# Kernel tuning notes

Measured on AMD Instinct MI355X. Metric: run time of the kernel, lower is better.

The kernel has to match this reference:

```python
import jax, jax.numpy as jnp
import numpy as np

TOPK_RATIO = 0.8


def setup_inputs() -> dict:
    key = jax.random.key(0)
    k1, k2, k3 = jax.random.split(key, 3)
    B, N, C = 32, 1024, 256
    x = jax.random.normal(k1, (B, N, C), dtype=jnp.float32)
    A = jax.random.uniform(k2, (B, N, N), dtype=jnp.float32)
    W = jax.random.normal(k3, (1, C), dtype=jnp.float32)  # nn.Linear(C, 1, bias=False).weight
    mask = jnp.ones((B, N), dtype=bool)                   # all nodes valid
    N_nodes = jnp.full((B,), N, dtype=jnp.int32)          # params_dict['N_nodes']
    return {"x": x, "A": A, "W": W, "mask": mask, "N_nodes": N_nodes}


def reference(x, A, W, mask, N_nodes):
    B, N, C = x.shape
    mask_f = mask.astype(x.dtype)
    n_nodes_f = N_nodes.astype(x.dtype)

    # unsup attention: alpha = normalize(exp(x @ W^T) * mask)
    alpha = jnp.exp(jnp.einsum('bnc,oc->bn', x, W)) * mask_f      # (B, N)
    alpha = alpha / (jnp.sum(alpha, axis=1, keepdims=True) + 1e-7)

    x = x * alpha[:, :, None]
    if N > 700:  # static shape condition, matches torch branch
        x = x * n_nodes_f[:, None, None]

    # top-k pooling: zero the mask of the N_remove lowest-alpha (valid) nodes
    N_remove = jnp.round(n_nodes_f * (1.0 - TOPK_RATIO)).astype(jnp.int32)  # (B,)
    order = jnp.argsort(alpha, axis=1)          # ascending alpha
    rank = jnp.argsort(order, axis=1)           # ascending rank per node
    new_mask = mask & (rank >= N_remove[:, None])  # all nodes valid => rank over valid set

    # drop_nodes_edges: gather the K kept nodes (static K since mask is full)
    K = N - int(round(N * (1.0 - TOPK_RATIO)))  # 819 for N=1024
    # score ranks valid nodes above invalid, earlier index first among valid
    score = new_mask.astype(jnp.int32) * (N + 1) - jnp.arange(N, dtype=jnp.int32)[None, :]
    _, idx = jax.lax.top_k(score, K)            # (B, K) kept node indices
    mask_kept = jnp.take_along_axis(new_mask, idx, axis=1)            # (B, K)
    x = jnp.take_along_axis(x, idx[:, :, None], axis=1)               # (B, K, C)
    A = jnp.take_along_axis(A, idx[:, :, None], axis=1)               # (B, K, N)
    A = jnp.take_along_axis(A, idx[:, None, :], axis=2)               # (B, K, K)

    mask_matrix = mask_kept[:, :, None] & mask_kept[:, None, :]
    A = A * mask_matrix.astype(A.dtype)
    return x, A, mask_kept, alpha
```

## Files before the change

### kernel.cpp

```cpp
#include <hip/hip_runtime.h>

#define B 32
#define N 1024
#define C 256
#define K 819
#define RPB 4
#define NROWGRP 205

__global__ __launch_bounds__(256) void k1_scores(const float* __restrict__ x,
                                                 const float* __restrict__ W,
                                                 float* __restrict__ y) {
    int row  = blockIdx.x * 4 + (threadIdx.x >> 6);
    int lane = threadIdx.x & 63;
    if (row >= B * N) return;
    const float4 xv = ((const float4*)(x + (size_t)row * C))[lane];
    const float4 wv = ((const float4*)W)[lane];
    float s = xv.x * wv.x + xv.y * wv.y + xv.z * wv.z + xv.w * wv.w;
    #pragma unroll
    for (int off = 32; off >= 1; off >>= 1)
        s += __shfl_down(s, off);
    if (lane == 0) y[row] = expf(s);
}

__global__ __launch_bounds__(1024) void k2_select(const float* __restrict__ y,
                                                  const int* __restrict__ N_nodes,
                                                  int* __restrict__ idx,
                                                  float* __restrict__ scale,
                                                  float* __restrict__ out_alpha,
                                                  float* __restrict__ out_mask) {
    __shared__ float a_sh[N];
    __shared__ float red[16];
    __shared__ int   wcnt[16];
    const int b    = blockIdx.x;
    const int i    = threadIdx.x;
    const int w    = i >> 6;
    const int lane = i & 63;

    float yi = y[b * N + i];

    float s = yi;
    #pragma unroll
    for (int off = 32; off >= 1; off >>= 1)
        s += __shfl_down(s, off);
    if (lane == 0) red[w] = s;
    __syncthreads();
    if (i == 0) {
        float S = 0.f;
        #pragma unroll
        for (int k = 0; k < 16; k++) S += red[k];
        red[0] = S + 1e-7f;
    }
    __syncthreads();
    const float denom = red[0];
    const float ai = yi / denom;
    a_sh[i] = ai;
    out_alpha[b * N + i] = ai;
    __syncthreads();

    int cnt = 0;
    for (int j = 0; j < N; j++) {
        float aj = a_sh[j];
        cnt += (int)((aj < ai) | ((aj == ai) & (j < i)));
    }

    const float nf = (float)N_nodes[b];
    const int nrem = (int)rintf(nf * (float)(1.0 - 0.8));
    const bool kept = (cnt >= nrem);

    unsigned long long bal = __ballot(kept);
    if (lane == 0) wcnt[w] = __popcll(bal);
    __syncthreads();
    int woff = 0;
    for (int k = 0; k < w; k++) woff += wcnt[k];
    if (kept) {
        int pos = woff + __popcll(bal & ((1ull << lane) - 1ull));
        idx[b * K + pos]      = i;
        scale[b * K + pos]    = ai * nf;
        out_mask[b * K + pos] = 1.0f;
    }
}

__global__ __launch_bounds__(256) void k3_gather_x(const float* __restrict__ x,
                                                   const int* __restrict__ idx,
                                                   const float* __restrict__ scale,
                                                   float* __restrict__ out_x) {
    const int bk = blockIdx.x;
    const int c  = threadIdx.x;
    const int b  = bk / K;
    const int node  = idx[bk];
    const float sc  = scale[bk];
    out_x[(size_t)bk * C + c] = x[((size_t)b * N + node) * C + c] * sc;
}

__global__ __launch_bounds__(256) void k4_gather_A(const float* __restrict__ A,
                                                   const int* __restrict__ idx,
                                                   float* __restrict__ out_A) {
    __shared__ int   idx_sh[K];
    __shared__ float rows[RPB][N];
    const int t  = threadIdx.x;
    const int b  = blockIdx.x / NROWGRP;
    const int i0 = (blockIdx.x % NROWGRP) * RPB;

    for (int j = t; j < K; j += 256) idx_sh[j] = idx[b * K + j];
    __syncthreads();

    #pragma unroll
    for (int r = 0; r < RPB; r++) {
        int i = i0 + r;
        if (i < K) {
            const float4* rp = (const float4*)(A + ((size_t)b * N + idx_sh[i]) * N);
            ((float4*)rows[r])[t] = rp[t];
        }
    }
    __syncthreads();

    #pragma unroll
    for (int r = 0; r < RPB; r++) {
        int i = i0 + r;
        if (i < K) {
            float* op = out_A + ((size_t)b * K + i) * K;
            for (int j = t; j < K; j += 256) op[j] = rows[r][idx_sh[j]];
        }
    }
}

extern "C" void kernel_launch(void* const* d_in, const int* in_sizes, int n_in,
                              void* d_out, int out_size, void* d_ws, size_t ws_size,
                              hipStream_t stream) {
    const float* x  = (const float*)d_in[0];
    const float* A  = (const float*)d_in[1];
    const float* W  = (const float*)d_in[2];
    const int* N_nodes = (const int*)d_in[4];

    float* out = (float*)d_out;
    const size_t x_sz = (size_t)B * K * C;
    const size_t A_sz = (size_t)B * K * K;
    const size_t m_sz = (size_t)B * K;
    float* out_x     = out;
    float* out_A     = out + x_sz;
    float* out_mask  = out + x_sz + A_sz;
    float* out_alpha = out + x_sz + A_sz + m_sz;

    float* y     = (float*)d_ws;
    int*   idx   = (int*)(y + (size_t)B * N);
    float* scale = (float*)(idx + (size_t)B * K);

    k1_scores<<<(B * N) / 4, 256, 0, stream>>>(x, W, y);
    k2_select<<<B, 1024, 0, stream>>>(y, N_nodes, idx, scale, out_alpha, out_mask);
    k3_gather_x<<<B * K, 256, 0, stream>>>(x, idx, scale, out_x);
    k4_gather_A<<<B * NROWGRP, 256, 0, stream>>>(A, idx, out_A);
}
```

Before: 301.3 us.

## Split ranking across more blocks and fuse x gather into A gather kernel

The single-block-per-batch select kernel is split in two. A rank kernel uses 4 blocks per batch and ranks on the raw exp scores, writing ballot bitmasks plus the per-batch sum. A small emit kernel then computes alpha and compacts the kept indices. The separate x-gather kernel, which used one tiny block per row, is folded into the A-gather kernel, and rows per block rise from 4 to 8. This adds a kernel launch and relies on ranking raw scores giving the same order as normalized alpha.

```diff
diff --git a/kernel.cpp b/kernel.cpp
--- a/kernel.cpp
+++ b/kernel.cpp
@@ -4,15 +4,14 @@
 #define N 1024
 #define C 256
 #define K 819
-#define RPB 4
-#define NROWGRP 205
+#define RPB 8
+#define NROWGRP 103
 
-__global__ __launch_bounds__(256) void k1_scores(const float* __restrict__ x,
+__global__ __launch_bounds__(256) void kA_scores(const float* __restrict__ x,
                                                  const float* __restrict__ W,
                                                  float* __restrict__ y) {
     int row  = blockIdx.x * 4 + (threadIdx.x >> 6);
     int lane = threadIdx.x & 63;
-    if (row >= B * N) return;
     const float4 xv = ((const float4*)(x + (size_t)row * C))[lane];
     const float4 wv = ((const float4*)W)[lane];
     float s = xv.x * wv.x + xv.y * wv.y + xv.z * wv.z + xv.w * wv.w;
@@ -22,101 +21,123 @@
     if (lane == 0) y[row] = expf(s);
 }
 
-__global__ __launch_bounds__(1024) void k2_select(const float* __restrict__ y,
-                                                  const int* __restrict__ N_nodes,
-                                                  int* __restrict__ idx,
-                                                  float* __restrict__ scale,
-                                                  float* __restrict__ out_alpha,
-                                                  float* __restrict__ out_mask) {
-    __shared__ float a_sh[N];
-    __shared__ float red[16];
-    __shared__ int   wcnt[16];
-    const int b    = blockIdx.x;
-    const int i    = threadIdx.x;
-    const int w    = i >> 6;
-    const int lane = i & 63;
+__global__ __launch_bounds__(256) void kB_rank(const float* __restrict__ y,
+                                               const int* __restrict__ N_nodes,
+                                               unsigned long long* __restrict__ bits,
+                                               float* __restrict__ denom) {
+    __shared__ float ysh[N];
+    __shared__ float red[4];
+    const int q = blockIdx.x;
+    const int b = blockIdx.y;
+    const int t = threadIdx.x;
+    const int w = t >> 6, lane = t & 63;
 
-    float yi = y[b * N + i];
-
-    float s = yi;
-    #pragma unroll
-    for (int off = 32; off >= 1; off >>= 1)
-        s += __shfl_down(s, off);
-    if (lane == 0) red[w] = s;
-    __syncthreads();
-    if (i == 0) {
-        float S = 0.f;
-        #pragma unroll
-        for (int k = 0; k < 16; k++) S += red[k];
-        red[0] = S + 1e-7f;
-    }
-    __syncthreads();
-    const float denom = red[0];
-    const float ai = yi / denom;
-    a_sh[i] = ai;
-    out_alpha[b * N + i] = ai;
+    ((float4*)ysh)[t] = ((const float4*)(y + (size_t)b * N))[t];
     __syncthreads();
 
+    const int i = q * 256 + t;
+    const float yi = ysh[i];
     int cnt = 0;
+    #pragma unroll 8
     for (int j = 0; j < N; j++) {
-        float aj = a_sh[j];
-        cnt += (int)((aj < ai) | ((aj == ai) & (j < i)));
+        float yj = ysh[j];
+        cnt += (int)((yj < yi) | ((yj == yi) & (j < i)));
     }
 
     const float nf = (float)N_nodes[b];
-    const int nrem = (int)rintf(nf * (float)(1.0 - 0.8));
+    const int nrem = (int)rintf(nf * 0.2f);
     const bool kept = (cnt >= nrem);
 
     unsigned long long bal = __ballot(kept);
-    if (lane == 0) wcnt[w] = __popcll(bal);
+    if (lane == 0) bits[b * 16 + q * 4 + w] = bal;
+
+    if (q == 0) {
+        float s = ysh[t] + ysh[t + 256] + ysh[t + 512] + ysh[t + 768];
+        #pragma unroll
+        for (int off = 32; off >= 1; off >>= 1)
+            s += __shfl_down(s, off);
+        if (lane == 0) red[w] = s;
+        __syncthreads();
+        if (t == 0) denom[b] = (red[0] + red[1] + red[2] + red[3]) + 1e-7f;
+    }
+}
+
+__global__ __launch_bounds__(1024) void kC_emit(const float* __restrict__ y,
+                                                const unsigned long long* __restrict__ bits,
+                                                const float* __restrict__ denom,
+                                                const int* __restrict__ N_nodes,
+                                                int* __restrict__ idx,
+                                                float* __restrict__ scale,
+                                                float* __restrict__ out_alpha,
+                                                float* __restrict__ out_mask) {
+    __shared__ unsigned long long w_sh[16];
+    __shared__ int c_sh[16];
+    const int b = blockIdx.x;
+    const int i = threadIdx.x;
+    if (i < 16) {
+        unsigned long long wv = bits[b * 16 + i];
+        w_sh[i] = wv;
+        c_sh[i] = __popcll(wv);
+    }
     __syncthreads();
-    int woff = 0;
-    for (int k = 0; k < w; k++) woff += wcnt[k];
-    if (kept) {
-        int pos = woff + __popcll(bal & ((1ull << lane) - 1ull));
+
+    const float d  = denom[b];
+    const float ai = y[b * N + i] / d;
+    out_alpha[b * N + i] = ai;
+
+    const int w = i >> 6, l = i & 63;
+    if ((w_sh[w] >> l) & 1ull) {
+        int pos = __popcll(w_sh[w] & ((1ull << l) - 1ull));
+        for (int k = 0; k < w; k++) pos += c_sh[k];
+        const float nf = (float)N_nodes[b];
         idx[b * K + pos]      = i;
         scale[b * K + pos]    = ai * nf;
         out_mask[b * K + pos] = 1.0f;
     }
 }
 
-__global__ __launch_bounds__(256) void k3_gather_x(const float* __restrict__ x,
-                                                   const int* __restrict__ idx,
-                                                   const float* __restrict__ scale,
-                                                   float* __restrict__ out_x) {
-    const int bk = blockIdx.x;
-    const int c  = threadIdx.x;
-    const int b  = bk / K;
-    const int node  = idx[bk];
-    const float sc  = scale[bk];
-    out_x[(size_t)bk * C + c] = x[((size_t)b * N + node) * C + c] * sc;
-}
-
-__global__ __launch_bounds__(256) void k4_gather_A(const float* __restrict__ A,
-                                                   const int* __restrict__ idx,
-                                                   float* __restrict__ out_A) {
+__global__ __launch_bounds__(256) void kD_gather(const float* __restrict__ A,
+                                                 const float* __restrict__ x,
+                                                 const int* __restrict__ idx,
+                                                 const float* __restrict__ scale,
+                                                 float* __restrict__ out_A,
+                                                 float* __restrict__ out_x) {
     __shared__ int   idx_sh[K];
     __shared__ float rows[RPB][N];
     const int t  = threadIdx.x;
-    const int b  = blockIdx.x / NROWGRP;
-    const int i0 = (blockIdx.x % NROWGRP) * RPB;
+    const int b  = blockIdx.y;
+    const int i0 = blockIdx.x * RPB;
 
     for (int j = t; j < K; j += 256) idx_sh[j] = idx[b * K + j];
-    __syncthreads();
 
     #pragma unroll
     for (int r = 0; r < RPB; r++) {
-        int i = i0 + r;
+        const int i = i0 + r;
         if (i < K) {
-            const float4* rp = (const float4*)(A + ((size_t)b * N + idx_sh[i]) * N);
+            const int node = idx[b * K + i];
+            const float4* rp = (const float4*)(A + ((size_t)b * N + node) * N);
             ((float4*)rows[r])[t] = rp[t];
+        }
+    }
+
+    #pragma unroll
+    for (int pass = 0; pass < 2; pass++) {
+        const int rr = pass * 4 + (t >> 6);
+        const int lane = t & 63;
+        const int i = i0 + rr;
+        if (i < K) {
+            const int   node = idx[b * K + i];
+            const float sc   = scale[b * K + i];
+            float4 v = ((const float4*)(x + ((size_t)b * N + node) * C))[lane];
+            v.x *= sc; v.y *= sc; v.z *= sc; v.w *= sc;
+            ((float4*)(out_x + ((size_t)b * K + i) * C))[lane] = v;
         }
     }
     __syncthreads();
 
     #pragma unroll
     for (int r = 0; r < RPB; r++) {
-        int i = i0 + r;
+        const int i = i0 + r;
         if (i < K) {
             float* op = out_A + ((size_t)b * K + i) * K;
             for (int j = t; j < K; j += 256) op[j] = rows[r][idx_sh[j]];
@@ -142,11 +163,13 @@
     float* out_alpha = out + x_sz + A_sz + m_sz;
 
     float* y     = (float*)d_ws;
-    int*   idx   = (int*)(y + (size_t)B * N);
+    unsigned long long* bits = (unsigned long long*)(y + (size_t)B * N);
+    float* denom = (float*)(bits + (size_t)B * 16);
+    int*   idx   = (int*)(denom + B);
     float* scale = (float*)(idx + (size_t)B * K);
 
-    k1_scores<<<(B * N) / 4, 256, 0, stream>>>(x, W, y);
-    k2_select<<<B, 1024, 0, stream>>>(y, N_nodes, idx, scale, out_alpha, out_mask);
-    k3_gather_x<<<B * K, 256, 0, stream>>>(x, idx, scale, out_x);
-    k4_gather_A<<<B * NROWGRP, 256, 0, stream>>>(A, idx, out_A);
+    kA_scores<<<(B * N) / 4, 256, 0, stream>>>(x, W, y);
+    kB_rank<<<dim3(4, B), 256, 0, stream>>>(y, N_nodes, bits, denom);
+    kC_emit<<<B, 1024, 0, stream>>>(y, bits, denom, N_nodes, idx, scale, out_alpha, out_mask);
+    kD_gather<<<dim3(NROWGRP, B), 256, 0, stream>>>(A, x, idx, scale, out_A, out_x);
 }
```

Measured after the change: 293.8 us. 2.5% less time.
